# Performance work log

Hardware: AMD Instinct MI355X
Metric: run time of the kernel (lower is better)

Reference implementation:

```python
import jax, jax.numpy as jnp
import numpy as np
import math

N_HEADS = 12


def setup_inputs() -> dict:
    key = jax.random.key(0)
    ks = jax.random.split(key, 6)
    B, S, DIM = 4, 2048, 768
    h = jax.random.normal(ks[0], (B, S, DIM), dtype=jnp.float32)
    attn_mask = jnp.ones((B, 1, 1, S), dtype=jnp.int32)
    scale = 1.0 / math.sqrt(DIM)
    wq = jax.random.normal(ks[1], (DIM, DIM), dtype=jnp.float32) * scale
    wk = jax.random.normal(ks[2], (DIM, DIM), dtype=jnp.float32) * scale
    wv = jax.random.normal(ks[3], (DIM, DIM), dtype=jnp.float32) * scale
    wo = jax.random.normal(ks[4], (DIM, DIM), dtype=jnp.float32) * scale
    return {"h": h, "attn_mask": attn_mask, "wq": wq, "wk": wk, "wv": wv, "wo": wo}


def reference(h, attn_mask, wq, wk, wv, wo):
    B, S, dim = h.shape
    H = N_HEADS
    D = dim // H
    qk_scale = 1.0 / math.sqrt(D)
    # NOTE: original uses .view(B, H, S, D) on the [B, S, H*D] projection —
    # a raw reshape, NOT the usual (B,S,H,D)->(B,H,S,D) transpose. Reproduce exactly.
    hq = (h @ wq.T).reshape(B, H, S, D)
    hk = (h @ wk.T).reshape(B, H, S, D)
    hv = (h @ wv.T).reshape(B, H, S, D)
    scores = jnp.einsum("bhqd,bhkd->bhqk", hq, hk) * qk_scale  # [B,H,S,S]
    scores = jnp.where(attn_mask == 0, -jnp.inf, scores)
    attn = jax.nn.softmax(scores.astype(jnp.float32), axis=-1)
    ctx = jnp.einsum("bhqk,bhkd->bhqd", attn, hv)  # [B,H,S,D]
    # dropout is identity in eval mode
    ctx = ctx.reshape(B, S, H * D)
    return ctx @ wo.T
```

## Files before the change

kernel.cpp:

```cpp
#include <hip/hip_runtime.h>
#include <math.h>

typedef __bf16 bf16x8 __attribute__((ext_vector_type(8)));
typedef float  f32x4  __attribute__((ext_vector_type(4)));
typedef float  f32x16 __attribute__((ext_vector_type(16)));

#define MFMA16(a, b, c) __builtin_amdgcn_mfma_f32_16x16x32_bf16((a), (b), (c), 0, 0, 0)
#define MFMA32(a, b, c) __builtin_amdgcn_mfma_f32_32x32x16_bf16((a), (b), (c), 0, 0, 0)

__device__ __forceinline__ unsigned short f2bf(float f) {
    unsigned int u = __float_as_uint(f);
    u += 0x7fffu + ((u >> 16) & 1u);
    return (unsigned short)(u >> 16);
}

__device__ __forceinline__ void gll16(const unsigned short* g, unsigned short* l) {
    __builtin_amdgcn_global_load_lds(
        (const __attribute__((address_space(1))) unsigned int*)g,
        (__attribute__((address_space(3))) unsigned int*)l, 16, 0, 0);
}

__global__ __launch_bounds__(256) void convert_kernel(
    const float* __restrict__ h, const float* __restrict__ wq,
    const float* __restrict__ wk, const float* __restrict__ wv,
    const float* __restrict__ wo,
    unsigned short* __restrict__ hb, unsigned short* __restrict__ wb)
{
    const int NH4 = 1572864;
    const int NW4 = 147456;
    int i4 = blockIdx.x * 256 + threadIdx.x;
    const float4* src;
    unsigned short* dst;
    int off;
    if (i4 < NH4) {
        src = (const float4*)h; dst = hb; off = i4;
    } else {
        int j = i4 - NH4;
        int w = j / NW4;
        off = j - w * NW4;
        const float* s = (w == 0) ? wq : (w == 1) ? wk : (w == 2) ? wv : wo;
        src = (const float4*)s;
        dst = wb + w * 589824;
    }
    float4 v = src[off];
    ushort4 o;
    o.x = f2bf(v.x); o.y = f2bf(v.y); o.z = f2bf(v.z); o.w = f2bf(v.w);
    ((ushort4*)dst)[off] = o;
}

template <typename OutT>
__global__ __launch_bounds__(256) void gemm_bt(
    const unsigned short* __restrict__ A,
    const unsigned short* __restrict__ Bm,
    OutT* __restrict__ C)
{
    constexpr int K = 768, N = 768;
    __shared__ unsigned short As[128 * 32];
    __shared__ unsigned short Bs[128 * 32];
    const unsigned short* Bz = Bm + (size_t)blockIdx.z * N * K;
    OutT* Cz = C + (size_t)blockIdx.z * 8192 * N;

    const int tid  = threadIdx.x;
    const int bm   = blockIdx.x * 128, bn = blockIdx.y * 128;
    const int wave = tid >> 6, lane = tid & 63;
    const int wm   = (wave & 1) * 64, wn = (wave >> 1) * 64;
    const int l16  = lane & 15, quad = lane >> 4;

    const int sr = tid >> 2, sp = (tid & 3) * 8;

    f32x4 acc[4][4] = {};

    for (int k0 = 0; k0 < K; k0 += 32) {
        __syncthreads();
        gll16(A  + (size_t)(bm + sr) * K      + k0 + sp, As + tid * 8);
        gll16(A  + (size_t)(bm + 64 + sr) * K + k0 + sp, As + 2048 + tid * 8);
        gll16(Bz + (size_t)(bn + sr) * K      + k0 + sp, Bs + tid * 8);
        gll16(Bz + (size_t)(bn + 64 + sr) * K + k0 + sp, Bs + 2048 + tid * 8);
        __syncthreads();

        bf16x8 af[4], bfv[4];
        #pragma unroll
        for (int i = 0; i < 4; i++)
            af[i] = *(const bf16x8*)(As + (wm + i * 16 + l16) * 32 + quad * 8);
        #pragma unroll
        for (int j = 0; j < 4; j++)
            bfv[j] = *(const bf16x8*)(Bs + (wn + j * 16 + l16) * 32 + quad * 8);
        #pragma unroll
        for (int i = 0; i < 4; i++)
            #pragma unroll
            for (int j = 0; j < 4; j++)
                acc[i][j] = MFMA16(af[i], bfv[j], acc[i][j]);
    }

    #pragma unroll
    for (int i = 0; i < 4; i++) {
        #pragma unroll
        for (int j = 0; j < 4; j++) {
            int row0 = bm + wm + i * 16 + quad * 4;
            int col  = bn + wn + j * 16 + l16;
            #pragma unroll
            for (int r = 0; r < 4; r++) {
                float v = acc[i][j][r];
                size_t idx = (size_t)(row0 + r) * N + col;
                if constexpr (sizeof(OutT) == 2) Cz[idx] = f2bf(v);
                else                             Cz[idx] = v;
            }
        }
    }
}

__global__ __launch_bounds__(256) void vtrans_kernel(
    const unsigned short* __restrict__ Vg,
    unsigned short* __restrict__ vt)
{
    constexpr int LDT = 72;
    __shared__ unsigned short Ts[64 * LDT];
    const int b = blockIdx.z, hh = blockIdx.y, kp0 = blockIdx.x * 64;
    const int tid = threadIdx.x;
    const size_t boff = (size_t)b * (24576 * 64);
    const int rowV0 = hh * 2048 + kp0;

    #pragma unroll
    for (int rep = 0; rep < 2; rep++) {
        int idx = rep * 256 + tid;
        int r = idx >> 3, dp = (idx & 7) * 8;
        uint4 v = *(const uint4*)(Vg + boff + (size_t)(rowV0 + r) * 64 + dp);
        unsigned short tmp[8];
        *(uint4*)tmp = v;
        #pragma unroll
        for (int i = 0; i < 8; i++) Ts[(dp + i) * LDT + r] = tmp[i];
    }
    __syncthreads();
    unsigned short* vtb = vt + ((size_t)(b * 12 + hh)) * 64 * 2048;
    #pragma unroll
    for (int rep = 0; rep < 2; rep++) {
        int idx = rep * 256 + tid;
        int d = idx >> 3, kp = (idx & 7) * 8;
        uint4 v = *(const uint4*)(Ts + d * LDT + kp);
        *(uint4*)(vtb + (size_t)d * 2048 + kp0 + kp) = v;
    }
}

__global__ __launch_bounds__(256) void attn_kernel(
    const unsigned short* __restrict__ Qg,
    const unsigned short* __restrict__ Kg,
    const unsigned short* __restrict__ vt,
    const int* __restrict__ mask,
    unsigned short* __restrict__ Og)
{
    __shared__ unsigned short Qs[128 * 64];
    __shared__ unsigned short Ks[64 * 64];
    __shared__ unsigned short Vs[64 * 64];

    const int b = blockIdx.z, hh = blockIdx.y, qt = blockIdx.x;
    const int tid  = threadIdx.x;
    const int wave = tid >> 6, lane = tid & 63;
    const int c31  = lane & 31, h = lane >> 5;
    const size_t boff = (size_t)b * (24576 * 64);
    const int rowQ0 = hh * 2048 + qt * 128;
    const int rowK0 = hh * 2048;
    const unsigned short* vtg = vt + ((size_t)(b * 12 + hh)) * 64 * 2048;
    const int sw = c31 & 7;

    #pragma unroll
    for (int i = 0; i < 4; i++) {
        int row = i * 32 + (tid >> 3);
        int ch  = (tid & 7) ^ (row & 7);
        gll16(Qg + boff + (size_t)(rowQ0 + row) * 64 + ch * 8, Qs + i * 2048 + tid * 8);
    }
    __syncthreads();

    bf16x8 qf[4];
    #pragma unroll
    for (int c = 0; c < 4; c++) {
        int ch = (2 * c + h) ^ sw;
        qf[c] = *(const bf16x8*)(Qs + (wave * 32 + c31) * 64 + ch * 8);
    }

    f32x16 acc[2] = {};
    float l_run = 0.f;

    for (int kt = 0; kt < 32; kt++) {
        __syncthreads();
        #pragma unroll
        for (int i = 0; i < 2; i++) {
            int row = i * 32 + (tid >> 3);
            int ch  = (tid & 7) ^ (row & 7);
            gll16(Kg  + boff + (size_t)(rowK0 + kt * 64 + row) * 64 + ch * 8,
                  Ks + i * 2048 + tid * 8);
            gll16(vtg + (size_t)row * 2048 + kt * 64 + ch * 8,
                  Vs + i * 2048 + tid * 8);
        }
        int4 mv[2][4];
        #pragma unroll
        for (int t2 = 0; t2 < 2; t2++)
            #pragma unroll
            for (int s = 0; s < 4; s++)
                mv[t2][s] = *(const int4*)(mask + b * 2048 + kt * 64 + t2 * 32 + 8 * s + 4 * h);
        __syncthreads();

        f32x16 sT[2];
        #pragma unroll
        for (int t2 = 0; t2 < 2; t2++) {
            f32x16 z = {};
            #pragma unroll
            for (int c = 0; c < 4; c++) {
                int ch = (2 * c + h) ^ sw;
                bf16x8 kf = *(const bf16x8*)(Ks + (t2 * 32 + c31) * 64 + ch * 8);
                z = MFMA32(kf, qf[c], z);
            }
            sT[t2] = z;
        }

        unsigned int p01[2][4], p23[2][4];
        #pragma unroll
        for (int t2 = 0; t2 < 2; t2++) {
            #pragma unroll
            for (int s = 0; s < 4; s++) {
                float e0 = __builtin_amdgcn_exp2f(sT[t2][4*s+0] * 0.18033688011112042f) * (float)mv[t2][s].x;
                float e1 = __builtin_amdgcn_exp2f(sT[t2][4*s+1] * 0.18033688011112042f) * (float)mv[t2][s].y;
                float e2 = __builtin_amdgcn_exp2f(sT[t2][4*s+2] * 0.18033688011112042f) * (float)mv[t2][s].z;
                float e3 = __builtin_amdgcn_exp2f(sT[t2][4*s+3] * 0.18033688011112042f) * (float)mv[t2][s].w;
                unsigned int u0 = __float_as_uint(e0) & 0xffff0000u;
                unsigned int u1 = __float_as_uint(e1) & 0xffff0000u;
                unsigned int u2 = __float_as_uint(e2) & 0xffff0000u;
                unsigned int u3 = __float_as_uint(e3) & 0xffff0000u;
                l_run += __uint_as_float(u0) + __uint_as_float(u1)
                       + __uint_as_float(u2) + __uint_as_float(u3);
                p01[t2][s] = __builtin_amdgcn_perm(u1, u0, 0x07060302u);
                p23[t2][s] = __builtin_amdgcn_perm(u3, u2, 0x07060302u);
            }
        }

        #pragma unroll
        for (int q = 0; q < 4; q++) {
            int t = q >> 1, p = q & 1;
            unsigned int L01 = h ? p01[t][2*p+1] : p01[t][2*p];
            unsigned int L23 = h ? p23[t][2*p+1] : p23[t][2*p];
            unsigned int pre01 = h ? p01[t][2*p] : p01[t][2*p+1];
            unsigned int pre23 = h ? p23[t][2*p] : p23[t][2*p+1];
            unsigned int P01 = (unsigned int)__shfl((int)pre01, lane ^ 32, 64);
            unsigned int P23 = (unsigned int)__shfl((int)pre23, lane ^ 32, 64);
            uint4 pfu;
            pfu.x = h ? P01 : L01;
            pfu.y = h ? P23 : L23;
            pfu.z = h ? L01 : P01;
            pfu.w = h ? L23 : P23;
            bf16x8 pf;
            __builtin_memcpy(&pf, &pfu, 16);
            #pragma unroll
            for (int nt = 0; nt < 2; nt++) {
                int ch = (2 * q + h) ^ sw;
                bf16x8 vf = *(const bf16x8*)(Vs + (nt * 32 + c31) * 64 + ch * 8);
                acc[nt] = MFMA32(pf, vf, acc[nt]);
            }
        }
    }

    float lt = l_run + __shfl_xor(l_run, 32, 64);
    float linv = 1.0f / lt;
    #pragma unroll
    for (int reg = 0; reg < 16; reg++) {
        int rowfn = (reg & 3) + 8 * (reg >> 2) + 4 * h;
        float li = __shfl(linv, rowfn, 64);
        int row = rowQ0 + wave * 32 + rowfn;
        #pragma unroll
        for (int nt = 0; nt < 2; nt++)
            Og[boff + (size_t)row * 64 + nt * 32 + c31] = f2bf(acc[nt][reg] * li);
    }
}

extern "C" void kernel_launch(void* const* d_in, const int* in_sizes, int n_in,
                              void* d_out, int out_size, void* d_ws, size_t ws_size,
                              hipStream_t stream)
{
    const float* h    = (const float*)d_in[0];
    const int*   mask = (const int*)d_in[1];
    const float* wq   = (const float*)d_in[2];
    const float* wk   = (const float*)d_in[3];
    const float* wv   = (const float*)d_in[4];
    const float* wo   = (const float*)d_in[5];

    unsigned short* hb  = (unsigned short*)d_ws;
    unsigned short* wb  = hb + 6291456;
    unsigned short* qkv = wb + 4 * 589824;
    unsigned short* ctx = qkv + (size_t)3 * 6291456;

    convert_kernel<<<8448, 256, 0, stream>>>(h, wq, wk, wv, wo, hb, wb);
    gemm_bt<unsigned short><<<dim3(64, 6, 3), 256, 0, stream>>>(hb, wb, qkv);
    vtrans_kernel<<<dim3(32, 12, 4), 256, 0, stream>>>(qkv + (size_t)2 * 6291456, hb);
    attn_kernel<<<dim3(16, 12, 4), 256, 0, stream>>>(
        qkv, qkv + 6291456, hb, mask, ctx);
    gemm_bt<float><<<dim3(64, 6, 1), 256, 0, stream>>>(
        ctx, wb + (size_t)3 * 589824, (float*)d_out);
}
```

Baseline: 266.8 us.

## Double-buffer LDS tiles in GEMM and attention kernels to overlap loads with MFMA

Both the projection GEMM and the attention kernel now use two LDS buffers, issuing the global-to-LDS load for the next K tile before computing on the current one. This removes one of the two barriers per iteration. The GEMM also gains an XOR swizzle on its 32-wide rows to reduce LDS bank conflicts on fragment reads. The cost is doubled LDS use, which may lower occupancy. Correctness relies on the single end-of-iteration barrier also covering completion of the async loads (vmcnt), which the compiler is expected to insert.

New measurement: 257.9 us. -3.3%, faster.

```diff
diff --git a/kernel.cpp b/kernel.cpp
--- a/kernel.cpp
+++ b/kernel.cpp
@@ -55,8 +55,8 @@
     OutT* __restrict__ C)
 {
     constexpr int K = 768, N = 768;
-    __shared__ unsigned short As[128 * 32];
-    __shared__ unsigned short Bs[128 * 32];
+    __shared__ unsigned short As[2][128 * 32];
+    __shared__ unsigned short Bs[2][128 * 32];
     const unsigned short* Bz = Bm + (size_t)blockIdx.z * N * K;
     OutT* Cz = C + (size_t)blockIdx.z * 8192 * N;
 
@@ -66,41 +66,51 @@
     const int wm   = (wave & 1) * 64, wn = (wave >> 1) * 64;
     const int l16  = lane & 15, quad = lane >> 4;
 
-    const int sr = tid >> 2, sp = (tid & 3) * 8;
+    const int sr  = tid >> 2;
+    const int sp8 = ((tid & 3) ^ (sr & 3)) * 8;
+    const int slot8 = (quad ^ (l16 & 3)) * 8;
+
+    auto stage = [&](int k0, int bi) {
+        gll16(A  + (size_t)(bm + sr) * K      + k0 + sp8, As[bi] + tid * 8);
+        gll16(A  + (size_t)(bm + 64 + sr) * K + k0 + sp8, As[bi] + 2048 + tid * 8);
+        gll16(Bz + (size_t)(bn + sr) * K      + k0 + sp8, Bs[bi] + tid * 8);
+        gll16(Bz + (size_t)(bn + 64 + sr) * K + k0 + sp8, Bs[bi] + 2048 + tid * 8);
+    };
 
     f32x4 acc[4][4] = {};
 
-    for (int k0 = 0; k0 < K; k0 += 32) {
+    stage(0, 0);
+    __syncthreads();
+
+    for (int i = 0; i < 24; i++) {
+        const int cur = i & 1;
+        if (i < 23) stage((i + 1) * 32, cur ^ 1);
+
+        bf16x8 af[4], bfv[4];
+        #pragma unroll
+        for (int ii = 0; ii < 4; ii++)
+            af[ii] = *(const bf16x8*)(As[cur] + (wm + ii * 16 + l16) * 32 + slot8);
+        #pragma unroll
+        for (int jj = 0; jj < 4; jj++)
+            bfv[jj] = *(const bf16x8*)(Bs[cur] + (wn + jj * 16 + l16) * 32 + slot8);
+        #pragma unroll
+        for (int ii = 0; ii < 4; ii++)
+            #pragma unroll
+            for (int jj = 0; jj < 4; jj++)
+                acc[ii][jj] = MFMA16(af[ii], bfv[jj], acc[ii][jj]);
+
         __syncthreads();
-        gll16(A  + (size_t)(bm + sr) * K      + k0 + sp, As + tid * 8);
-        gll16(A  + (size_t)(bm + 64 + sr) * K + k0 + sp, As + 2048 + tid * 8);
-        gll16(Bz + (size_t)(bn + sr) * K      + k0 + sp, Bs + tid * 8);
-        gll16(Bz + (size_t)(bn + 64 + sr) * K + k0 + sp, Bs + 2048 + tid * 8);
-        __syncthreads();
-
-        bf16x8 af[4], bfv[4];
-        #pragma unroll
-        for (int i = 0; i < 4; i++)
-            af[i] = *(const bf16x8*)(As + (wm + i * 16 + l16) * 32 + quad * 8);
-        #pragma unroll
-        for (int j = 0; j < 4; j++)
-            bfv[j] = *(const bf16x8*)(Bs + (wn + j * 16 + l16) * 32 + quad * 8);
-        #pragma unroll
-        for (int i = 0; i < 4; i++)
-            #pragma unroll
-            for (int j = 0; j < 4; j++)
-                acc[i][j] = MFMA16(af[i], bfv[j], acc[i][j]);
-    }
-
-    #pragma unroll
-    for (int i = 0; i < 4; i++) {
-        #pragma unroll
-        for (int j = 0; j < 4; j++) {
-            int row0 = bm + wm + i * 16 + quad * 4;
-            int col  = bn + wn + j * 16 + l16;
+    }
+
+    #pragma unroll
+    for (int ii = 0; ii < 4; ii++) {
+        #pragma unroll
+        for (int jj = 0; jj < 4; jj++) {
+            int row0 = bm + wm + ii * 16 + quad * 4;
+            int col  = bn + wn + jj * 16 + l16;
             #pragma unroll
             for (int r = 0; r < 4; r++) {
-                float v = acc[i][j][r];
+                float v = acc[ii][jj][r];
                 size_t idx = (size_t)(row0 + r) * N + col;
                 if constexpr (sizeof(OutT) == 2) Cz[idx] = f2bf(v);
                 else                             Cz[idx] = v;
@@ -149,8 +159,8 @@
     unsigned short* __restrict__ Og)
 {
     __shared__ unsigned short Qs[128 * 64];
-    __shared__ unsigned short Ks[64 * 64];
-    __shared__ unsigned short Vs[64 * 64];
+    __shared__ unsigned short Ks[2][64 * 64];
+    __shared__ unsigned short Vs[2][64 * 64];
 
     const int b = blockIdx.z, hh = blockIdx.y, qt = blockIdx.x;
     const int tid  = threadIdx.x;
@@ -162,12 +172,26 @@
     const unsigned short* vtg = vt + ((size_t)(b * 12 + hh)) * 64 * 2048;
     const int sw = c31 & 7;
 
+    const int srow = tid >> 3;
+    const int sch8 = ((tid & 7) ^ (srow & 7)) * 8;
+
+    auto stageKV = [&](int kt, int bi) {
+        #pragma unroll
+        for (int i = 0; i < 2; i++) {
+            int row = i * 32 + srow;
+            gll16(Kg  + boff + (size_t)(rowK0 + kt * 64 + row) * 64 + sch8,
+                  Ks[bi] + i * 2048 + tid * 8);
+            gll16(vtg + (size_t)row * 2048 + kt * 64 + sch8,
+                  Vs[bi] + i * 2048 + tid * 8);
+        }
+    };
+
     #pragma unroll
     for (int i = 0; i < 4; i++) {
-        int row = i * 32 + (tid >> 3);
-        int ch  = (tid & 7) ^ (row & 7);
-        gll16(Qg + boff + (size_t)(rowQ0 + row) * 64 + ch * 8, Qs + i * 2048 + tid * 8);
-    }
+        int row = i * 32 + srow;
+        gll16(Qg + boff + (size_t)(rowQ0 + row) * 64 + sch8, Qs + i * 2048 + tid * 8);
+    }
+    stageKV(0, 0);
     __syncthreads();
 
     bf16x8 qf[4];
@@ -181,23 +205,15 @@
     float l_run = 0.f;
 
     for (int kt = 0; kt < 32; kt++) {
-        __syncthreads();
-        #pragma unroll
-        for (int i = 0; i < 2; i++) {
-            int row = i * 32 + (tid >> 3);
-            int ch  = (tid & 7) ^ (row & 7);
-            gll16(Kg  + boff + (size_t)(rowK0 + kt * 64 + row) * 64 + ch * 8,
-                  Ks + i * 2048 + tid * 8);
-            gll16(vtg + (size_t)row * 2048 + kt * 64 + ch * 8,
-                  Vs + i * 2048 + tid * 8);
-        }
+        const int cur = kt & 1;
+        if (kt < 31) stageKV(kt + 1, cur ^ 1);
+
         int4 mv[2][4];
         #pragma unroll
         for (int t2 = 0; t2 < 2; t2++)
             #pragma unroll
             for (int s = 0; s < 4; s++)
                 mv[t2][s] = *(const int4*)(mask + b * 2048 + kt * 64 + t2 * 32 + 8 * s + 4 * h);
-        __syncthreads();
 
         f32x16 sT[2];
         #pragma unroll
@@ -206,7 +222,7 @@
             #pragma unroll
             for (int c = 0; c < 4; c++) {
                 int ch = (2 * c + h) ^ sw;
-                bf16x8 kf = *(const bf16x8*)(Ks + (t2 * 32 + c31) * 64 + ch * 8);
+                bf16x8 kf = *(const bf16x8*)(Ks[cur] + (t2 * 32 + c31) * 64 + ch * 8);
                 z = MFMA32(kf, qf[c], z);
             }
             sT[t2] = z;
@@ -251,10 +267,12 @@
             #pragma unroll
             for (int nt = 0; nt < 2; nt++) {
                 int ch = (2 * q + h) ^ sw;
-                bf16x8 vf = *(const bf16x8*)(Vs + (nt * 32 + c31) * 64 + ch * 8);
+                bf16x8 vf = *(const bf16x8*)(Vs[cur] + (nt * 32 + c31) * 64 + ch * 8);
                 acc[nt] = MFMA32(pf, vf, acc[nt]);
             }
         }
+
+        __syncthreads();
     }
 
     float lt = l_run + __shfl_xor(l_run, 32, 64);
```
